# Optimization experiments

Hardware: AMD Instinct MI355X
Metric: run time of the kernel (lower is better)

The kernel has to match this reference:

```python
import jax, jax.numpy as jnp
import numpy as np

POOL = 7; SR = 2; SCALE = 1.0 / 16
NUM_CLASSES = 21
NMS_THR = 0.5; MIN_SIZE = 1.0; TOPK = 100; SCORE_THR = 0.05
BBOX_CLIP = float(np.log(1000.0 / 16))


def roi_align(feat, rois):
    # feat: [C,H,W]; rois: [P,4] xyxy in image coords. torchvision aligned=True, sampling_ratio=2.
    C, H, W = feat.shape
    S = POOL * SR
    x0r = rois[:, 0] * SCALE - 0.5
    y0r = rois[:, 1] * SCALE - 0.5
    bw = (rois[:, 2] - rois[:, 0]) * SCALE / POOL
    bh = (rois[:, 3] - rois[:, 1]) * SCALE / POOL
    t = (jnp.arange(S, dtype=feat.dtype) + 0.5) / SR  # sample offsets in bin units
    ys = y0r[:, None] + bh[:, None] * t  # [P,S]
    xs = x0r[:, None] + bw[:, None] * t  # [P,S]
    vy = (ys >= -1.0) & (ys <= H)
    vx = (xs >= -1.0) & (xs <= W)
    y = jnp.clip(ys, 0.0, H - 1)
    x = jnp.clip(xs, 0.0, W - 1)
    yl = jnp.floor(y).astype(jnp.int32); xl = jnp.floor(x).astype(jnp.int32)
    yh = jnp.minimum(yl + 1, H - 1);     xh = jnp.minimum(xl + 1, W - 1)
    ly = y - yl; lx = x - xl
    hy = 1.0 - ly; hx = 1.0 - lx

    def g(Yi, Xi):  # -> [C,P,S,S]
        return feat[:, Yi[:, :, None], Xi[:, None, :]]

    val = (g(yl, xl) * (hy[:, :, None] * hx[:, None, :])
         + g(yl, xh) * (hy[:, :, None] * lx[:, None, :])
         + g(yh, xl) * (ly[:, :, None] * hx[:, None, :])
         + g(yh, xh) * (ly[:, :, None] * lx[:, None, :]))
    val = val * (vy[:, :, None] & vx[:, None, :])[None].astype(feat.dtype)
    P = rois.shape[0]
    val = val.reshape(C, P, POOL, SR, POOL, SR).mean(axis=(3, 5))  # avg over 2x2 samples/bin
    return val.transpose(1, 0, 2, 3)  # [P,C,POOL,POOL]


def decode(pred, proposals):
    # pred: [N,K,4] (dx,dy,dw,dh); proposals: [N,4]
    w = proposals[:, 2] - proposals[:, 0]
    h = proposals[:, 3] - proposals[:, 1]
    cx = proposals[:, 0] + 0.5 * w
    cy = proposals[:, 1] + 0.5 * h
    dx, dy = pred[..., 0], pred[..., 1]
    dw = jnp.minimum(pred[..., 2], BBOX_CLIP)
    dh = jnp.minimum(pred[..., 3], BBOX_CLIP)
    pcx = dx * w[:, None] + cx[:, None]
    pcy = dy * h[:, None] + cy[:, None]
    pw = jnp.exp(dw) * w[:, None]
    ph = jnp.exp(dh) * h[:, None]
    return jnp.stack([pcx - 0.5 * pw, pcy - 0.5 * ph, pcx + 0.5 * pw, pcy + 0.5 * ph], axis=-1)


def box_iou(b):
    x1, y1, x2, y2 = b[:, 0], b[:, 1], b[:, 2], b[:, 3]
    area = (x2 - x1) * (y2 - y1)
    iw = jnp.maximum(jnp.minimum(x2[:, None], x2[None, :]) - jnp.maximum(x1[:, None], x1[None, :]), 0.0)
    ih = jnp.maximum(jnp.minimum(y2[:, None], y2[None, :]) - jnp.maximum(y1[:, None], y1[None, :]), 0.0)
    inter = iw * ih
    return inter / (area[:, None] + area[None, :] - inter)


def filter_predictions(boxes, labels, scores):
    # score threshold + min-size + per-class greedy NMS + topK, static shapes (padded to TOPK)
    N = scores.shape[0]
    ws = boxes[:, 2] - boxes[:, 0]
    hs = boxes[:, 3] - boxes[:, 1]
    valid = (scores > SCORE_THR) & (ws >= MIN_SIZE) & (hs >= MIN_SIZE)
    skey = jnp.where(valid, scores, -jnp.inf)
    order = jnp.argsort(-skey)
    b = boxes[order]; s = skey[order]; l = labels[order]; v = valid[order]
    # batched_nms via per-class coordinate offset
    off = jax.lax.stop_gradient(jnp.max(boxes) + 1.0)
    ob = jax.lax.stop_gradient(b) + (l.astype(b.dtype) * off)[:, None]
    iou = box_iou(ob)  # [N,N]
    idx = jnp.arange(N)

    def body(keep, i):
        sup = (iou[i] > NMS_THR) & keep[i] & (idx > i)
        return keep & ~sup, None

    keep, _ = jax.lax.scan(body, v, idx)
    rank = jnp.cumsum(keep) - 1
    final = keep & (rank < TOPK)
    pick = jnp.argsort(jnp.where(final, idx, N))[:TOPK]  # kept indices in score order, padded
    ok = final[pick]
    out_boxes = jnp.where(ok[:, None], b[pick], 0.0)
    out_scores = jnp.where(ok, s[pick], 0.0)
    out_labels = jnp.where(ok, l[pick], -1)
    return out_boxes, out_labels, out_scores


def roi_head_forward(image, feat, proposals, fc6_w, fc6_b, fc7_w, fc7_b, cls_w, cls_b, reg_w, reg_b):
    H_img, W_img = image.shape[-2], image.shape[-1]
    pooled = roi_align(feat[0], proposals)  # [P,C,7,7]
    x = pooled.reshape(pooled.shape[0], -1)
    x = jax.nn.relu(x @ fc6_w.T + fc6_b)
    x = jax.nn.relu(x @ fc7_w.T + fc7_b)
    cls_scores = x @ cls_w.T + cls_b                       # [P,K]
    box_pred = (x @ reg_w.T + reg_b).reshape(-1, NUM_CLASSES, 4)
    boxes = decode(box_pred, proposals)                    # [P,K,4]
    scores = jax.nn.softmax(cls_scores, axis=-1)
    boxes = jnp.stack([boxes[..., 0].clip(0, W_img), boxes[..., 1].clip(0, H_img),
                       boxes[..., 2].clip(0, W_img), boxes[..., 3].clip(0, H_img)], axis=-1)
    labels = jnp.broadcast_to(jnp.arange(NUM_CLASSES), scores.shape)
    boxes = boxes[:, 1:].reshape(-1, 4)
    scores = scores[:, 1:].reshape(-1)
    labels = (labels[:, 1:] - 1).reshape(-1)
    return filter_predictions(boxes, labels, scores)


def setup_inputs() -> dict:
    key = jax.random.key(0)
    ks = jax.random.split(key, 12)
    H_img, W_img = 800, 1072
    P, C = 300, 512
    image = jnp.zeros((1, 3, H_img, W_img), jnp.float32)
    feat = jax.random.normal(ks[0], (1, C, H_img // 16, W_img // 16), jnp.float32)
    cx = jax.random.uniform(ks[1], (P,)) * W_img
    cy = jax.random.uniform(ks[2], (P,)) * H_img
    bw = 20.0 + jax.random.uniform(ks[3], (P,)) * 300.0
    bh = 20.0 + jax.random.uniform(ks[4], (P,)) * 300.0
    proposals = jnp.stack([jnp.clip(cx - bw / 2, 0, W_img), jnp.clip(cy - bh / 2, 0, H_img),
                           jnp.clip(cx + bw / 2, 0, W_img), jnp.clip(cy + bh / 2, 0, H_img)], axis=1)
    fin = C * POOL * POOL  # 25088
    D = 1024
    fc6_w = jax.random.normal(ks[5], (D, fin), jnp.float32) / np.sqrt(fin)
    fc6_b = jnp.zeros((D,), jnp.float32)
    fc7_w = jax.random.normal(ks[6], (D, D), jnp.float32) / np.sqrt(D)
    fc7_b = jnp.zeros((D,), jnp.float32)
    cls_w = jax.random.normal(ks[7], (NUM_CLASSES, D), jnp.float32) / np.sqrt(D)
    cls_b = jnp.zeros((NUM_CLASSES,), jnp.float32)
    reg_w = jax.random.normal(ks[8], (NUM_CLASSES * 4, D), jnp.float32) * 0.001
    reg_b = jnp.zeros((NUM_CLASSES * 4,), jnp.float32)
    return {"image": image, "feat": feat, "proposals": proposals,
            "fc6_w": fc6_w, "fc6_b": fc6_b, "fc7_w": fc7_w, "fc7_b": fc7_b,
            "cls_w": cls_w, "cls_b": cls_b, "reg_w": reg_w, "reg_b": reg_b}


def reference(image, feat, proposals, fc6_w, fc6_b, fc7_w, fc7_b, cls_w, cls_b, reg_w, reg_b):
    return roi_head_forward(image, feat, proposals, fc6_w, fc6_b, fc7_w, fc7_b, cls_w, cls_b, reg_w, reg_b)
```

## Files before the change

kernel.cpp:

```cpp
#include <hip/hip_runtime.h>
#include <hip/hip_bf16.h>
#include <math.h>

#define P_N   300
#define C_N   512
#define H_F   50
#define W_F   67
#define HW_F  3350
#define D_N   1024
#define FIN   25088
#define NCLS  21
#define NCAND 6000
#define W_IMG 1072.0f
#define H_IMG 800.0f
#define BBOX_CLIP_F 4.135166556742356f
#define KS6   40
#define STEPS6_PER_Z 20
#define KS7   16
#define STEPS7_PER_Z 2
#define KSH   16
#define STEPSH_PER_Z 2
#define NHEAD 128
#define NW    96
#define A_SCALE 16.0f
#define B_SCALE 256.0f
#define O_SCALE (1.0f / 4096.0f)
#define TBLK  1680

typedef __attribute__((ext_vector_type(8)))  _Float16 half8;
typedef __attribute__((ext_vector_type(16))) float    f32x16;

__device__ __forceinline__ void splitA(float f, _Float16& h, _Float16& l) {
  float fs = f * A_SCALE;
  h = (_Float16)fs;
  l = (_Float16)(fs - (float)h);
}

__global__ __launch_bounds__(256) void prep_transpose(const float* __restrict__ feat,
                                                      float* __restrict__ ft,
                                                      const float* __restrict__ cls_w,
                                                      const float* __restrict__ cls_b,
                                                      const float* __restrict__ reg_w,
                                                      const float* __restrict__ reg_b,
                                                      float* __restrict__ Wpad,
                                                      float* __restrict__ bpad,
                                                      int* __restrict__ vcount) {
  __shared__ float tile[32][33];
  const int bid = blockIdx.x;
  const int tid = threadIdx.x;
  if (bid < TBLK) {
    const int bx = bid % 105, byy = bid / 105;
    const int s0 = bx * 32, c0 = byy * 32;
    const int tx = tid & 31, ty = tid >> 5;
    for (int r = ty; r < 32; r += 8) {
      int c = c0 + r, s = s0 + tx;
      tile[r][tx] = (s < HW_F) ? feat[(size_t)c * HW_F + s] : 0.0f;
    }
    __syncthreads();
    for (int r = ty; r < 32; r += 8) {
      int s = s0 + r, c = c0 + tx;
      if (s < HW_F) ft[(size_t)s * C_N + c] = tile[tx][r];
    }
  } else {
    const int row = bid - TBLK;
    if (row == 0 && tid == 0) *vcount = 0;
    const float* src = (row < NCLS) ? (cls_w + (size_t)row * D_N)
                     : (row < 105)  ? (reg_w + (size_t)(row - NCLS) * D_N) : nullptr;
    float4 v = make_float4(0.f, 0.f, 0.f, 0.f);
    if (src) v = reinterpret_cast<const float4*>(src)[tid];
    reinterpret_cast<float4*>(Wpad + (size_t)row * D_N)[tid] = v;
    if (tid == 0)
      bpad[row] = (row < NCLS) ? cls_b[row] : (row < 105) ? reg_b[row - NCLS] : 0.0f;
  }
}

__global__ __launch_bounds__(256) void roi_align_k(const float* __restrict__ ft,
                                                   const float* __restrict__ rois,
                                                   _Float16* __restrict__ Xhi,
                                                   _Float16* __restrict__ Xlo) {
  __shared__ _Float16 hbuf[12544] __attribute__((aligned(16)));
  __shared__ _Float16 lbuf[12544] __attribute__((aligned(16)));
  __shared__ int   g_yl[14], g_yh[14], g_xl[14], g_xh[14];
  __shared__ float g_ly[14], g_hy[14], g_lx[14], g_hx[14];
  __shared__ int   g_vy[14], g_vx[14];

  const int p   = blockIdx.x;
  const int ch  = blockIdx.y;
  const int tid = threadIdx.x;

  if (tid < 14) {
    const float rx0 = rois[p*4+0], ry0 = rois[p*4+1], rx1 = rois[p*4+2], ry1 = rois[p*4+3];
    const float x0r = rx0 * 0.0625f - 0.5f;
    const float y0r = ry0 * 0.0625f - 0.5f;
    const float bw  = (rx1 - rx0) * 0.0625f * (1.0f / 7.0f);
    const float bh  = (ry1 - ry0) * 0.0625f * (1.0f / 7.0f);
    const float t   = ((float)tid + 0.5f) * 0.5f;

    const float ys = y0r + bh * t;
    g_vy[tid] = (ys >= -1.0f) && (ys <= (float)H_F);
    float y = fminf(fmaxf(ys, 0.0f), (float)(H_F - 1));
    int yi = (int)floorf(y);
    g_yl[tid] = yi; g_yh[tid] = min(yi + 1, H_F - 1);
    g_ly[tid] = y - (float)yi; g_hy[tid] = 1.0f - (y - (float)yi);

    const float xs = x0r + bw * t;
    g_vx[tid] = (xs >= -1.0f) && (xs <= (float)W_F);
    float x = fminf(fmaxf(xs, 0.0f), (float)(W_F - 1));
    int xi = (int)floorf(x);
    g_xl[tid] = xi; g_xh[tid] = min(xi + 1, W_F - 1);
    g_lx[tid] = x - (float)xi; g_hx[tid] = 1.0f - (x - (float)xi);
  }
  __syncthreads();

  const int c = ch * 256 + tid;
  for (int cell = 0; cell < 49; ++cell) {
    const int py = cell / 7;
    const int px = cell - py * 7;
    float acc = 0.0f;
#pragma unroll
    for (int sy = 0; sy < 2; ++sy) {
      const int iy = 2 * py + sy;
      if (!g_vy[iy]) continue;
      const float ly = g_ly[iy], hy = g_hy[iy];
      const int ry0i = g_yl[iy] * W_F, ry1i = g_yh[iy] * W_F;
#pragma unroll
      for (int sx = 0; sx < 2; ++sx) {
        const int ix = 2 * px + sx;
        if (!g_vx[ix]) continue;
        const float lx = g_lx[ix], hx = g_hx[ix];
        const float* b00 = ft + (size_t)(ry0i + g_xl[ix]) * C_N;
        const float* b01 = ft + (size_t)(ry0i + g_xh[ix]) * C_N;
        const float* b10 = ft + (size_t)(ry1i + g_xl[ix]) * C_N;
        const float* b11 = ft + (size_t)(ry1i + g_xh[ix]) * C_N;
        acc += (hy*hx)*b00[c] + (hy*lx)*b01[c] + (ly*hx)*b10[c] + (ly*lx)*b11[c];
      }
    }
    _Float16 h, l;
    splitA(acc * 0.25f, h, l);
    hbuf[tid * 49 + cell] = h;
    lbuf[tid * 49 + cell] = l;
  }
  __syncthreads();

  const size_t base = (size_t)p * FIN + (size_t)ch * 12544;
  const uint4* hs = (const uint4*)hbuf;
  const uint4* ls = (const uint4*)lbuf;
  uint4* dh = (uint4*)(Xhi + base);
  uint4* dl = (uint4*)(Xlo + base);
  for (int k = tid; k < 1568; k += 256) { dh[k] = hs[k]; dl[k] = ls[k]; }
}

__device__ __forceinline__ int swz(int slot, int ks) {
  return slot ^ ((slot >> 5) & 1) ^ (((slot >> 3) & 1) << 1) ^ ((ks & 1) << 2);
}

__global__ __launch_bounds__(256, 3) void gemm_f16_3p(
    const _Float16* __restrict__ Ahi, const _Float16* __restrict__ Alo,
    const float* __restrict__ Wt, float* __restrict__ Pt,
    int M, int K, int steps_per_z, int ldc)
{
  __shared__ _Float16 lds[20480];
  const int tid  = threadIdx.x;
  const int lane = tid & 63, wave = tid >> 6;
  const int wm = wave >> 1, wn = wave & 1;

  const int GX = gridDim.x, GY = gridDim.y;
  const int T  = GX * GY * gridDim.z;
  int flat = blockIdx.x + GX * (blockIdx.y + GY * blockIdx.z);
  if ((T & 7) == 0) flat = (flat & 7) * (T >> 3) + (flat >> 3);
  const int bx = flat % GX;
  const int by = (flat / GX) % GY;
  const int bz = flat / (GX * GY);

  const int m0 = bx * 192, n0 = by * 128;
  const int steps_total = K >> 5;
  const int s0 = bz * steps_per_z;
  const int s1 = min(s0 + steps_per_z, steps_total);

  f32x16 acc[3][2];
#pragma unroll
  for (int a = 0; a < 3; ++a)
#pragma unroll
    for (int b = 0; b < 2; ++b)
#pragma unroll
      for (int r = 0; r < 16; ++r) acc[a][b][r] = 0.f;

  const int srow = tid >> 2;
  const int j8   = tid & 3;
  const int ksW  = j8 >> 1, kc8 = j8 & 1;
  const int wslot = swz((kc8 << 5) | (srow & 31), ksW);

  for (int step = s0; step < s1; ++step) {
    const int kb = step << 5;
#pragma unroll
    for (int half = 0; half < 3; ++half) {
      const int row = srow + half * 64;
      const int mf  = row >> 5;
      const int gm  = m0 + row;
      uint4 vh = make_uint4(0,0,0,0), vl = make_uint4(0,0,0,0);
      if (gm < M) {
        vh = *reinterpret_cast<const uint4*>(Ahi + (size_t)gm * K + kb + j8 * 8);
        vl = *reinterpret_cast<const uint4*>(Alo + (size_t)gm * K + kb + j8 * 8);
      }
      const int base = (mf * 2 + ksW) * 512 + wslot * 8;
      *reinterpret_cast<uint4*>(&lds[base])        = vh;
      *reinterpret_cast<uint4*>(&lds[6144 + base]) = vl;
    }
#pragma unroll
    for (int half = 0; half < 2; ++half) {
      const int n = srow + half * 64;
      const float* wp = Wt + (size_t)(n0 + n) * K + kb + j8 * 8;
      const float4 f0 = *reinterpret_cast<const float4*>(wp);
      const float4 f1 = *reinterpret_cast<const float4*>(wp + 4);
      float fv[8] = {f0.x, f0.y, f0.z, f0.w, f1.x, f1.y, f1.z, f1.w};
      union { _Float16 h[8]; uint4 v; } uh, ul;
#pragma unroll
      for (int e = 0; e < 8; ++e) {
        float fs = fv[e] * B_SCALE;
        uh.h[e] = (_Float16)fs;
        ul.h[e] = (_Float16)(fs - (float)uh.h[e]);
      }
      const int nf = n >> 5;
      const int base = 12288 + (nf * 2 + ksW) * 512 + wslot * 8;
      *reinterpret_cast<uint4*>(&lds[base])        = uh.v;
      *reinterpret_cast<uint4*>(&lds[4096 + base]) = ul.v;
    }
    __syncthreads();
#pragma unroll
    for (int ks = 0; ks < 2; ++ks) {
      const int rslot = swz(lane, ks) * 8;
      half8 ah[3], al[3], bh[2], bl[2];
#pragma unroll
      for (int mi = 0; mi < 3; ++mi) {
        const int mf = wm * 3 + mi;
        ah[mi] = *reinterpret_cast<const half8*>(&lds[(mf * 2 + ks) * 512 + rslot]);
        al[mi] = *reinterpret_cast<const half8*>(&lds[6144 + (mf * 2 + ks) * 512 + rslot]);
      }
#pragma unroll
      for (int ni = 0; ni < 2; ++ni) {
        const int nf = wn * 2 + ni;
        bh[ni] = *reinterpret_cast<const half8*>(&lds[12288 + (nf * 2 + ks) * 512 + rslot]);
        bl[ni] = *reinterpret_cast<const half8*>(&lds[16384 + (nf * 2 + ks) * 512 + rslot]);
      }
#pragma unroll
      for (int mi = 0; mi < 3; ++mi)
#pragma unroll
        for (int ni = 0; ni < 2; ++ni) {
          acc[mi][ni] = __builtin_amdgcn_mfma_f32_32x32x16_f16(ah[mi], bh[ni], acc[mi][ni], 0, 0, 0);
          acc[mi][ni] = __builtin_amdgcn_mfma_f32_32x32x16_f16(ah[mi], bl[ni], acc[mi][ni], 0, 0, 0);
          acc[mi][ni] = __builtin_amdgcn_mfma_f32_32x32x16_f16(al[mi], bh[ni], acc[mi][ni], 0, 0, 0);
        }
    }
    __syncthreads();
  }
  const int col = lane & 31, rhi = lane >> 5;
  float* outp = Pt + (size_t)bz * ((size_t)M * ldc);
#pragma unroll
  for (int mi = 0; mi < 3; ++mi)
#pragma unroll
    for (int ni = 0; ni < 2; ++ni) {
      const int n = n0 + (wn * 2 + ni) * 32 + col;
      if (n >= ldc) continue;
#pragma unroll
      for (int r = 0; r < 16; ++r) {
        const int m = m0 + (wm * 3 + mi) * 32 + ((r & 3) + 8 * (r >> 2) + 4 * rhi);
        if (m < M) outp[(size_t)m * ldc + n] = acc[mi][ni][r] * O_SCALE;
      }
    }
}

__global__ __launch_bounds__(256) void reduce_bias(
    const float* __restrict__ Pt, const float* __restrict__ bias,
    float* __restrict__ out_f32, _Float16* __restrict__ out_hi, _Float16* __restrict__ out_lo,
    int MN, int KS, int nmask, int relu)
{
  int i = blockIdx.x * 256 + threadIdx.x;
  if (i >= MN) return;
  float s = 0.0f;
  for (int k = 0; k < KS; ++k) s += Pt[(size_t)k * MN + i];
  s += bias[i & nmask];
  if (relu) s = fmaxf(s, 0.0f);
  if (out_f32) out_f32[i] = s;
  if (out_hi) {
    _Float16 h, l; splitA(s, h, l);
    out_hi[i] = h; out_lo[i] = l;
  }
}

__global__ __launch_bounds__(64) void decode_kernel(const float* __restrict__ logits,
                                                    const float* __restrict__ props,
                                                    float* __restrict__ cboxes,
                                                    unsigned long long* __restrict__ ckeys,
                                                    int* __restrict__ vcount) {
  const int p = blockIdx.x;
  const int lane = threadIdx.x;
  const float* lg = logits + (size_t)p * NHEAD;

  float s = (lane < NCLS) ? lg[lane] : -__builtin_inff();
  float mx = s;
#pragma unroll
  for (int off = 32; off > 0; off >>= 1) mx = fmaxf(mx, __shfl_xor(mx, off));
  float e = (lane < NCLS) ? expf(s - mx) : 0.0f;
  float sum = e;
#pragma unroll
  for (int off = 32; off > 0; off >>= 1) sum += __shfl_xor(sum, off);
  const float sm = e / sum;

  if (lane >= 1 && lane < NCLS) {
    const int c = lane;
    const float x0 = props[p*4+0], y0 = props[p*4+1], x1 = props[p*4+2], y1 = props[p*4+3];
    const float w = x1 - x0, hh = y1 - y0;
    const float cx = x0 + 0.5f * w, cy = y0 + 0.5f * hh;
    const float dx = lg[NCLS + c*4 + 0];
    const float dy = lg[NCLS + c*4 + 1];
    const float dw = fminf(lg[NCLS + c*4 + 2], BBOX_CLIP_F);
    const float dh = fminf(lg[NCLS + c*4 + 3], BBOX_CLIP_F);
    const float pcx = dx * w + cx, pcy = dy * hh + cy;
    const float pw = expf(dw) * w, ph = expf(dh) * hh;
    float bx0 = pcx - 0.5f * pw, by0 = pcy - 0.5f * ph;
    float bx1 = pcx + 0.5f * pw, by1 = pcy + 0.5f * ph;
    bx0 = fminf(fmaxf(bx0, 0.0f), W_IMG);
    by0 = fminf(fmaxf(by0, 0.0f), H_IMG);
    bx1 = fminf(fmaxf(bx1, 0.0f), W_IMG);
    by1 = fminf(fmaxf(by1, 0.0f), H_IMG);
    const int idx = p * 20 + (c - 1);
    cboxes[idx*4+0] = bx0; cboxes[idx*4+1] = by0;
    cboxes[idx*4+2] = bx1; cboxes[idx*4+3] = by1;
    const bool valid = (sm > 0.05f) && ((bx1 - bx0) >= 1.0f) && ((by1 - by0) >= 1.0f);
    if (valid) {
      int pos = atomicAdd(vcount, 1);
      unsigned u = __float_as_uint(sm);
      ckeys[pos] = ((unsigned long long)(~u) << 32) | (unsigned)idx;
    }
  }
}

__global__ __launch_bounds__(1024) void sort_gather(const unsigned long long* __restrict__ ckeys,
                                                    const int* __restrict__ vcount,
                                                    const float* __restrict__ cboxes,
                                                    float4* __restrict__ sbox,
                                                    float* __restrict__ sscore,
                                                    int* __restrict__ slab) {
  __shared__ unsigned long long keys[8192];
  const int tid = threadIdx.x;
  const int V = *vcount;
  int Npad = 64; while (Npad < V) Npad <<= 1;
  for (int i = tid; i < Npad; i += 1024)
    keys[i] = (i < V) ? ckeys[i] : ~0ULL;
  __syncthreads();
  for (int kk = 2; kk <= Npad; kk <<= 1) {
    for (int j = kk >> 1; j > 0; j >>= 1) {
      for (int i = tid; i < Npad; i += 1024) {
        int ij = i ^ j;
        if (ij > i) {
          unsigned long long a = keys[i], b = keys[ij];
          bool up = ((i & kk) == 0);
          if ((a > b) == up) { keys[i] = b; keys[ij] = a; }
        }
      }
      __syncthreads();
    }
  }
  for (int i = tid; i < V; i += 1024) {
    unsigned long long key = keys[i];
    int idx = (int)(key & 0xffffffffu);
    sbox[i]   = *reinterpret_cast<const float4*>(&cboxes[(size_t)idx * 4]);
    sscore[i] = __uint_as_float(~(unsigned)(key >> 32));
    slab[i]   = idx % 20;
  }
}

__global__ __launch_bounds__(256) void iou_matrix(const float4* __restrict__ sbox,
                                                  const int* __restrict__ slab,
                                                  const int* __restrict__ vcount,
                                                  unsigned long long* __restrict__ mask) {
  const int V = *vcount;
  const int i = blockIdx.x * 4 + (threadIdx.x >> 6);
  const int lane = threadIdx.x & 63;
  if (i >= V) return;
  const float4 bi = sbox[i];
  const int li = slab[i];
  const float ai = (bi.z - bi.x) * (bi.w - bi.y);
  const int nw = (V + 63) >> 6;
  for (int w = 0; w < nw; ++w) {
    const int j = (w << 6) + lane;
    bool sup = false;
    if (j > i && j < V && slab[j] == li) {
      const float4 bj = sbox[j];
      const float iw = fminf(bi.z, bj.z) - fmaxf(bi.x, bj.x);
      const float ih = fminf(bi.w, bj.w) - fmaxf(bi.y, bj.y);
      const float inter = fmaxf(iw, 0.0f) * fmaxf(ih, 0.0f);
      const float aj = (bj.z - bj.x) * (bj.w - bj.y);
      sup = inter / (ai + aj - inter) > 0.5f;
    }
    const unsigned long long m = __ballot(sup);
    if (lane == 0) mask[(size_t)i * NW + w] = m;
  }
}

__device__ __forceinline__ unsigned long long bcast_live(unsigned long long live0,
                                                         unsigned long long live1, int w) {
  union { unsigned long long u; uint2 v; } t;
  t.u = (w < 64) ? live0 : live1;
  const int src = w & 63;
  const unsigned lo = __shfl(t.v.x, src);
  const unsigned hi = __shfl(t.v.y, src);
  return ((unsigned long long)hi << 32) | lo;
}

__global__ __launch_bounds__(64) void nms_scan(const float4* __restrict__ sbox,
                                               const float* __restrict__ sscore,
                                               const int* __restrict__ slab,
                                               const int* __restrict__ vcount,
                                               const unsigned long long* __restrict__ mask,
                                               float* __restrict__ out) {
  const int lane = threadIdx.x;
  const int V = min(*vcount, NCAND);
  const int nw = (V + 63) >> 6;
  unsigned long long live0 = ~0ULL, live1 = ~0ULL;
  int nk = 0;
  for (int w = 0; w < nw && nk < 100; ++w) {
    const int nb = V - (w << 6);
    const unsigned long long vmask = (nb >= 64) ? ~0ULL : ((1ULL << nb) - 1ULL);
    unsigned long long wv = bcast_live(live0, live1, w) & vmask;
    while (wv && nk < 100) {
      const int b = __ffsll((long long)wv) - 1;
      const int i = (w << 6) + b;
      if (lane == 0) {
        const float4 bb = sbox[i];
        out[nk*4+0] = bb.x; out[nk*4+1] = bb.y; out[nk*4+2] = bb.z; out[nk*4+3] = bb.w;
        out[400 + nk] = (float)slab[i];
        out[500 + nk] = sscore[i];
      }
      const unsigned long long* mrow = mask + (size_t)i * NW;
      if (lane < nw) live0 &= ~mrow[lane];
      if (64 + lane < nw) live1 &= ~mrow[64 + lane];
      nk++;
      wv = bcast_live(live0, live1, w) & vmask;
      wv &= (b == 63) ? 0ULL : ~((2ULL << b) - 1ULL);
    }
  }
  for (int r = nk + lane; r < 100; r += 64) {
    out[r*4+0] = 0.0f; out[r*4+1] = 0.0f; out[r*4+2] = 0.0f; out[r*4+3] = 0.0f;
    out[400 + r] = -1.0f;
    out[500 + r] = 0.0f;
  }
}

extern "C" void kernel_launch(void* const* d_in, const int* in_sizes, int n_in,
                              void* d_out, int out_size, void* d_ws, size_t ws_size,
                              hipStream_t stream) {
  const float* feat   = (const float*)d_in[1];
  const float* props  = (const float*)d_in[2];
  const float* fc6_w  = (const float*)d_in[3];
  const float* fc6_b  = (const float*)d_in[4];
  const float* fc7_w  = (const float*)d_in[5];
  const float* fc7_b  = (const float*)d_in[6];
  const float* cls_w  = (const float*)d_in[7];
  const float* cls_b  = (const float*)d_in[8];
  const float* reg_w  = (const float*)d_in[9];
  const float* reg_b  = (const float*)d_in[10];

  char* ws = (char*)d_ws;
  size_t off = 0;
  auto alloc = [&](size_t bytes) -> void* {
    void* p = ws + off;
    off += (bytes + 255) & ~(size_t)255;
    return p;
  };

  _Float16* Xhi  = (_Float16*)alloc((size_t)P_N * FIN * 2);
  _Float16* Xlo  = (_Float16*)alloc((size_t)P_N * FIN * 2);
  float*    Pt   = (float*)alloc((size_t)KS6 * P_N * D_N * 4);
  _Float16* h6hi = (_Float16*)alloc((size_t)P_N * D_N * 2);
  _Float16* h6lo = (_Float16*)alloc((size_t)P_N * D_N * 2);
  _Float16* h7hi = (_Float16*)alloc((size_t)P_N * D_N * 2);
  _Float16* h7lo = (_Float16*)alloc((size_t)P_N * D_N * 2);
  float*    Wpad = (float*)alloc((size_t)NHEAD * D_N * 4);
  float*    bpad = (float*)alloc((size_t)NHEAD * 4);
  float*  logits = (float*)alloc((size_t)P_N * NHEAD * 4);
  float*  cboxes = (float*)alloc((size_t)NCAND * 4 * 4);
  unsigned long long* ckeys = (unsigned long long*)alloc((size_t)NCAND * 8);
  float4*   sbox = (float4*)alloc((size_t)NCAND * 16);
  float*  sscore = (float*)alloc((size_t)NCAND * 4);
  int*      slab = (int*)alloc((size_t)NCAND * 4);
  unsigned long long* supmask = (unsigned long long*)alloc((size_t)NCAND * NW * 8);
  int*    vcount = (int*)alloc(256);
  float* ft = Pt;
  (void)ws_size; (void)in_sizes; (void)n_in; (void)out_size;

  prep_transpose<<<TBLK + NHEAD, 256, 0, stream>>>(feat, ft, cls_w, cls_b, reg_w, reg_b,
                                                   Wpad, bpad, vcount);
  roi_align_k<<<dim3(P_N, 2), 256, 0, stream>>>(ft, props, Xhi, Xlo);
  gemm_f16_3p<<<dim3(2, 8, KS6), 256, 0, stream>>>(Xhi, Xlo, fc6_w, Pt, P_N, FIN, STEPS6_PER_Z, D_N);
  reduce_bias<<<(P_N * D_N + 255) / 256, 256, 0, stream>>>(
      Pt, fc6_b, nullptr, h6hi, h6lo, P_N * D_N, KS6, D_N - 1, 1);
  gemm_f16_3p<<<dim3(2, 8, KS7), 256, 0, stream>>>(h6hi, h6lo, fc7_w, Pt, P_N, D_N, STEPS7_PER_Z, D_N);
  reduce_bias<<<(P_N * D_N + 255) / 256, 256, 0, stream>>>(
      Pt, fc7_b, nullptr, h7hi, h7lo, P_N * D_N, KS7, D_N - 1, 1);
  gemm_f16_3p<<<dim3(2, 1, KSH), 256, 0, stream>>>(h7hi, h7lo, Wpad, Pt, P_N, D_N, STEPSH_PER_Z, NHEAD);
  reduce_bias<<<(P_N * NHEAD + 255) / 256, 256, 0, stream>>>(
      Pt, bpad, logits, nullptr, nullptr, P_N * NHEAD, KSH, NHEAD - 1, 0);
  decode_kernel<<<P_N, 64, 0, stream>>>(logits, props, cboxes, ckeys, vcount);
  sort_gather<<<1, 1024, 0, stream>>>(ckeys, vcount, cboxes, sbox, sscore, slab);
  iou_matrix<<<(NCAND + 3) / 4, 256, 0, stream>>>(sbox, slab, vcount, supmask);
  nms_scan<<<1, 64, 0, stream>>>(sbox, sscore, slab, vcount, supmask, (float*)d_out);
}
```

Before: 343.9 us.

## Pre-swizzle GEMM A operands into LDS-ready blobs and load via global_load_lds

Adds a reshuffle kernel that packs the ROI-aligned fp16 hi/lo activations into per-tile, per-k-step 16KB blobs already in the swizzled LDS layout. The GEMM then copies A straight into LDS with global_load_lds instead of doing per-thread loads and stores. The reduction kernels for fc6 and fc7 now write their outputs directly in this blob format. The M tile shrinks from 192 to 128 (a 3-wide grid), fc6 split-K goes from 40 to 28 slices, and the workspace is reorganised so buffers alias. The cost is an extra reshuffle pass over the roughly 30MB activation buffer, plus fewer accumulators per wave.

```diff
diff --git a/kernel.cpp b/kernel.cpp
--- a/kernel.cpp
+++ b/kernel.cpp
@@ -14,8 +14,8 @@
 #define W_IMG 1072.0f
 #define H_IMG 800.0f
 #define BBOX_CLIP_F 4.135166556742356f
-#define KS6   40
-#define STEPS6_PER_Z 20
+#define KS6   28
+#define STEPS6_PER_Z 28
 #define KS7   16
 #define STEPS7_PER_Z 2
 #define KSH   16
@@ -34,6 +34,16 @@
   float fs = f * A_SCALE;
   h = (_Float16)fs;
   l = (_Float16)(fs - (float)h);
+}
+
+__device__ __forceinline__ int swz(int slot, int ks) {
+  return slot ^ ((slot >> 5) & 1) ^ (((slot >> 3) & 1) << 1) ^ ((ks & 1) << 2);
+}
+
+__device__ __forceinline__ int blob_half_idx(int row, int j8) {
+  const int ksW = j8 >> 1, kc8 = j8 & 1;
+  const int mf = row >> 5;
+  return (mf * 2 + ksW) * 512 + swz((kc8 << 5) | (row & 31), ksW) * 8;
 }
 
 __global__ __launch_bounds__(256) void prep_transpose(const float* __restrict__ feat,
@@ -150,16 +160,40 @@
   for (int k = tid; k < 1568; k += 256) { dh[k] = hs[k]; dl[k] = ls[k]; }
 }
 
-__device__ __forceinline__ int swz(int slot, int ks) {
-  return slot ^ ((slot >> 5) & 1) ^ (((slot >> 3) & 1) << 1) ^ ((ks & 1) << 2);
+__global__ __launch_bounds__(256) void reshuffle_x(const _Float16* __restrict__ Shi,
+                                                   const _Float16* __restrict__ Slo,
+                                                   char* __restrict__ blob,
+                                                   int M2, int K) {
+  __shared__ _Float16 buf[8192] __attribute__((aligned(16)));
+  const int tile = blockIdx.x, step = blockIdx.y;
+  const int tid = threadIdx.x;
+  const int steps = K >> 5;
+#pragma unroll
+  for (int i = 0; i < 4; ++i) {
+    const int g = tid + i * 256;
+    const int half = g >> 9;
+    const int row = (g >> 2) & 127;
+    const int j8 = g & 3;
+    const int gm = tile * 128 + row;
+    uint4 v = make_uint4(0, 0, 0, 0);
+    if (gm < M2) {
+      const _Float16* src = (half ? Slo : Shi) + (size_t)gm * K + (step << 5) + (j8 << 3);
+      v = *reinterpret_cast<const uint4*>(src);
+    }
+    *reinterpret_cast<uint4*>(buf + half * 4096 + blob_half_idx(row, j8)) = v;
+  }
+  __syncthreads();
+  uint4* dst = (uint4*)(blob + (((size_t)tile * steps + step) << 14));
+  const uint4* s = (const uint4*)buf;
+#pragma unroll
+  for (int i = 0; i < 4; ++i) dst[tid + i * 256] = s[tid + i * 256];
 }
 
 __global__ __launch_bounds__(256, 3) void gemm_f16_3p(
-    const _Float16* __restrict__ Ahi, const _Float16* __restrict__ Alo,
-    const float* __restrict__ Wt, float* __restrict__ Pt,
+    const char* __restrict__ Ablob, const float* __restrict__ Wt, float* __restrict__ Pt,
     int M, int K, int steps_per_z, int ldc)
 {
-  __shared__ _Float16 lds[20480];
+  __shared__ _Float16 lds[16384] __attribute__((aligned(16)));
   const int tid  = threadIdx.x;
   const int lane = tid & 63, wave = tid >> 6;
   const int wm = wave >> 1, wn = wave & 1;
@@ -172,14 +206,14 @@
   const int by = (flat / GX) % GY;
   const int bz = flat / (GX * GY);
 
-  const int m0 = bx * 192, n0 = by * 128;
+  const int m0 = bx * 128, n0 = by * 128;
   const int steps_total = K >> 5;
   const int s0 = bz * steps_per_z;
   const int s1 = min(s0 + steps_per_z, steps_total);
 
-  f32x16 acc[3][2];
-#pragma unroll
-  for (int a = 0; a < 3; ++a)
+  f32x16 acc[2][2];
+#pragma unroll
+  for (int a = 0; a < 2; ++a)
 #pragma unroll
     for (int b = 0; b < 2; ++b)
 #pragma unroll
@@ -192,19 +226,14 @@
 
   for (int step = s0; step < s1; ++step) {
     const int kb = step << 5;
-#pragma unroll
-    for (int half = 0; half < 3; ++half) {
-      const int row = srow + half * 64;
-      const int mf  = row >> 5;
-      const int gm  = m0 + row;
-      uint4 vh = make_uint4(0,0,0,0), vl = make_uint4(0,0,0,0);
-      if (gm < M) {
-        vh = *reinterpret_cast<const uint4*>(Ahi + (size_t)gm * K + kb + j8 * 8);
-        vl = *reinterpret_cast<const uint4*>(Alo + (size_t)gm * K + kb + j8 * 8);
-      }
-      const int base = (mf * 2 + ksW) * 512 + wslot * 8;
-      *reinterpret_cast<uint4*>(&lds[base])        = vh;
-      *reinterpret_cast<uint4*>(&lds[6144 + base]) = vl;
+    const char* Ab = Ablob + (((size_t)bx * steps_total + step) << 14);
+#pragma unroll
+    for (int c2 = 0; c2 < 4; ++c2) {
+      const int off = ((wave << 2) + c2) << 10;
+      __builtin_amdgcn_global_load_lds(
+          (const __attribute__((address_space(1))) uint32_t*)(Ab + off + (lane << 4)),
+          (__attribute__((address_space(3))) uint32_t*)((char*)lds + off),
+          16, 0, 0);
     }
 #pragma unroll
     for (int half = 0; half < 2; ++half) {
@@ -221,7 +250,7 @@
         ul.h[e] = (_Float16)(fs - (float)uh.h[e]);
       }
       const int nf = n >> 5;
-      const int base = 12288 + (nf * 2 + ksW) * 512 + wslot * 8;
+      const int base = 8192 + (nf * 2 + ksW) * 512 + wslot * 8;
       *reinterpret_cast<uint4*>(&lds[base])        = uh.v;
       *reinterpret_cast<uint4*>(&lds[4096 + base]) = ul.v;
     }
@@ -229,21 +258,21 @@
 #pragma unroll
     for (int ks = 0; ks < 2; ++ks) {
       const int rslot = swz(lane, ks) * 8;
-      half8 ah[3], al[3], bh[2], bl[2];
-#pragma unroll
-      for (int mi = 0; mi < 3; ++mi) {
-        const int mf = wm * 3 + mi;
+      half8 ah[2], al[2], bh[2], bl[2];
+#pragma unroll
+      for (int mi = 0; mi < 2; ++mi) {
+        const int mf = wm * 2 + mi;
         ah[mi] = *reinterpret_cast<const half8*>(&lds[(mf * 2 + ks) * 512 + rslot]);
-        al[mi] = *reinterpret_cast<const half8*>(&lds[6144 + (mf * 2 + ks) * 512 + rslot]);
+        al[mi] = *reinterpret_cast<const half8*>(&lds[4096 + (mf * 2 + ks) * 512 + rslot]);
       }
 #pragma unroll
       for (int ni = 0; ni < 2; ++ni) {
         const int nf = wn * 2 + ni;
-        bh[ni] = *reinterpret_cast<const half8*>(&lds[12288 + (nf * 2 + ks) * 512 + rslot]);
-        bl[ni] = *reinterpret_cast<const half8*>(&lds[16384 + (nf * 2 + ks) * 512 + rslot]);
-      }
-#pragma unroll
-      for (int mi = 0; mi < 3; ++mi)
+        bh[ni] = *reinterpret_cast<const half8*>(&lds[8192  + (nf * 2 + ks) * 512 + rslot]);
+        bl[ni] = *reinterpret_cast<const half8*>(&lds[12288 + (nf * 2 + ks) * 512 + rslot]);
+      }
+#pragma unroll
+      for (int mi = 0; mi < 2; ++mi)
 #pragma unroll
         for (int ni = 0; ni < 2; ++ni) {
           acc[mi][ni] = __builtin_amdgcn_mfma_f32_32x32x16_f16(ah[mi], bh[ni], acc[mi][ni], 0, 0, 0);
@@ -256,35 +285,63 @@
   const int col = lane & 31, rhi = lane >> 5;
   float* outp = Pt + (size_t)bz * ((size_t)M * ldc);
 #pragma unroll
-  for (int mi = 0; mi < 3; ++mi)
+  for (int mi = 0; mi < 2; ++mi)
 #pragma unroll
     for (int ni = 0; ni < 2; ++ni) {
       const int n = n0 + (wn * 2 + ni) * 32 + col;
       if (n >= ldc) continue;
 #pragma unroll
       for (int r = 0; r < 16; ++r) {
-        const int m = m0 + (wm * 3 + mi) * 32 + ((r & 3) + 8 * (r >> 2) + 4 * rhi);
+        const int m = m0 + (wm * 2 + mi) * 32 + ((r & 3) + 8 * (r >> 2) + 4 * rhi);
         if (m < M) outp[(size_t)m * ldc + n] = acc[mi][ni][r] * O_SCALE;
       }
     }
 }
 
-__global__ __launch_bounds__(256) void reduce_bias(
-    const float* __restrict__ Pt, const float* __restrict__ bias,
-    float* __restrict__ out_f32, _Float16* __restrict__ out_hi, _Float16* __restrict__ out_lo,
-    int MN, int KS, int nmask, int relu)
-{
+__global__ __launch_bounds__(256) void reduce_frag(const float* __restrict__ Pt,
+                                                   const float* __restrict__ bias,
+                                                   char* __restrict__ blob,
+                                                   int KS, int stepsB) {
+  const int g = blockIdx.x * 256 + threadIdx.x;
+  if (g >= P_N * 128) return;
+  const int m = g >> 7;
+  const int gg = g & 127;
+  const int n0 = gg << 3;
+  float s[8];
+#pragma unroll
+  for (int e = 0; e < 8; ++e) s[e] = bias[n0 + e];
+  for (int k2 = 0; k2 < KS; ++k2) {
+    const float* pp = Pt + ((size_t)k2 * P_N + m) * D_N + n0;
+    const float4 a = *reinterpret_cast<const float4*>(pp);
+    const float4 b = *reinterpret_cast<const float4*>(pp + 4);
+    s[0]+=a.x; s[1]+=a.y; s[2]+=a.z; s[3]+=a.w;
+    s[4]+=b.x; s[5]+=b.y; s[6]+=b.z; s[7]+=b.w;
+  }
+  union { _Float16 h[8]; uint4 v; } uh, ul;
+#pragma unroll
+  for (int e = 0; e < 8; ++e) {
+    float r = fmaxf(s[e], 0.0f);
+    _Float16 h, l; splitA(r, h, l);
+    uh.h[e] = h; ul.h[e] = l;
+  }
+  const int tile = m >> 7, row = m & 127;
+  const int step = gg >> 2, j8 = gg & 3;
+  _Float16* dst = (_Float16*)(blob + (((size_t)tile * stepsB + step) << 14));
+  const int hidx = blob_half_idx(row, j8);
+  *reinterpret_cast<uint4*>(dst + hidx) = uh.v;
+  *reinterpret_cast<uint4*>(dst + 4096 + hidx) = ul.v;
+}
+
+__global__ __launch_bounds__(256) void reduce_bias(const float* __restrict__ Pt,
+                                                   const float* __restrict__ bias,
+                                                   float* __restrict__ out_f32,
+                                                   int MN, int KS, int nmask) {
   int i = blockIdx.x * 256 + threadIdx.x;
   if (i >= MN) return;
   float s = 0.0f;
   for (int k = 0; k < KS; ++k) s += Pt[(size_t)k * MN + i];
   s += bias[i & nmask];
-  if (relu) s = fmaxf(s, 0.0f);
-  if (out_f32) out_f32[i] = s;
-  if (out_hi) {
-    _Float16 h, l; splitA(s, h, l);
-    out_hi[i] = h; out_lo[i] = l;
-  }
+  out_f32[i] = s;
 }
 
 __global__ __launch_bounds__(64) void decode_kernel(const float* __restrict__ logits,
@@ -462,45 +519,46 @@
   const float* reg_b  = (const float*)d_in[10];
 
   char* ws = (char*)d_ws;
-  size_t off = 0;
+  const size_t XSZ = (size_t)P_N * FIN * 2;
+  const size_t R1  = (size_t)KS6 * P_N * D_N * 4;
+  _Float16* Xhi = (_Float16*)ws;
+  _Float16* Xlo = (_Float16*)(ws + XSZ);
+  float*    Pt  = (float*)ws;
+  char* reg2 = ws + R1;
+  float* ft   = (float*)reg2;
+  char*  Xb   = reg2;
+  const size_t XBSZ = (size_t)3 * 784 * 16384;
+  size_t off = R1 + XBSZ;
   auto alloc = [&](size_t bytes) -> void* {
     void* p = ws + off;
     off += (bytes + 255) & ~(size_t)255;
     return p;
   };
-
-  _Float16* Xhi  = (_Float16*)alloc((size_t)P_N * FIN * 2);
-  _Float16* Xlo  = (_Float16*)alloc((size_t)P_N * FIN * 2);
-  float*    Pt   = (float*)alloc((size_t)KS6 * P_N * D_N * 4);
-  _Float16* h6hi = (_Float16*)alloc((size_t)P_N * D_N * 2);
-  _Float16* h6lo = (_Float16*)alloc((size_t)P_N * D_N * 2);
-  _Float16* h7hi = (_Float16*)alloc((size_t)P_N * D_N * 2);
-  _Float16* h7lo = (_Float16*)alloc((size_t)P_N * D_N * 2);
-  float*    Wpad = (float*)alloc((size_t)NHEAD * D_N * 4);
-  float*    bpad = (float*)alloc((size_t)NHEAD * 4);
-  float*  logits = (float*)alloc((size_t)P_N * NHEAD * 4);
-  float*  cboxes = (float*)alloc((size_t)NCAND * 4 * 4);
+  char*  h6b   = (char*)alloc((size_t)3 * 32 * 16384);
+  char*  h7b   = (char*)alloc((size_t)3 * 32 * 16384);
+  float* Wpad  = (float*)alloc((size_t)NHEAD * D_N * 4);
+  float* bpad  = (float*)alloc((size_t)NHEAD * 4);
+  float* logits= (float*)alloc((size_t)P_N * NHEAD * 4);
+  float* cboxes= (float*)alloc((size_t)NCAND * 4 * 4);
   unsigned long long* ckeys = (unsigned long long*)alloc((size_t)NCAND * 8);
-  float4*   sbox = (float4*)alloc((size_t)NCAND * 16);
-  float*  sscore = (float*)alloc((size_t)NCAND * 4);
-  int*      slab = (int*)alloc((size_t)NCAND * 4);
+  float4* sbox = (float4*)alloc((size_t)NCAND * 16);
+  float* sscore= (float*)alloc((size_t)NCAND * 4);
+  int*   slab  = (int*)alloc((size_t)NCAND * 4);
   unsigned long long* supmask = (unsigned long long*)alloc((size_t)NCAND * NW * 8);
-  int*    vcount = (int*)alloc(256);
-  float* ft = Pt;
+  int*   vcount= (int*)alloc(256);
   (void)ws_size; (void)in_sizes; (void)n_in; (void)out_size;
 
   prep_transpose<<<TBLK + NHEAD, 256, 0, stream>>>(feat, ft, cls_w, cls_b, reg_w, reg_b,
                                                    Wpad, bpad, vcount);
   roi_align_k<<<dim3(P_N, 2), 256, 0, stream>>>(ft, props, Xhi, Xlo);
-  gemm_f16_3p<<<dim3(2, 8, KS6), 256, 0, stream>>>(Xhi, Xlo, fc6_w, Pt, P_N, FIN, STEPS6_PER_Z, D_N);
-  reduce_bias<<<(P_N * D_N + 255) / 256, 256, 0, stream>>>(
-      Pt, fc6_b, nullptr, h6hi, h6lo, P_N * D_N, KS6, D_N - 1, 1);
-  gemm_f16_3p<<<dim3(2, 8, KS7), 256, 0, stream>>>(h6hi, h6lo, fc7_w, Pt, P_N, D_N, STEPS7_PER_Z, D_N);
-  reduce_bias<<<(P_N * D_N + 255) / 256, 256, 0, stream>>>(
-      Pt, fc7_b, nullptr, h7hi, h7lo, P_N * D_N, KS7, D_N - 1, 1);
-  gemm_f16_3p<<<dim3(2, 1, KSH), 256, 0, stream>>>(h7hi, h7lo, Wpad, Pt, P_N, D_N, STEPSH_PER_Z, NHEAD);
+  reshuffle_x<<<dim3(3, 784), 256, 0, stream>>>(Xhi, Xlo, Xb, P_N, FIN);
+  gemm_f16_3p<<<dim3(3, 8, KS6), 256, 0, stream>>>(Xb, fc6_w, Pt, P_N, FIN, STEPS6_PER_Z, D_N);
+  reduce_frag<<<150, 256, 0, stream>>>(Pt, fc6_b, h6b, KS6, 32);
+  gemm_f16_3p<<<dim3(3, 8, KS7), 256, 0, stream>>>(h6b, fc7_w, Pt, P_N, D_N, STEPS7_PER_Z, D_N);
+  reduce_frag<<<150, 256, 0, stream>>>(Pt, fc7_b, h7b, KS7, 32);
+  gemm_f16_3p<<<dim3(3, 1, KSH), 256, 0, stream>>>(h7b, Wpad, Pt, P_N, D_N, STEPSH_PER_Z, NHEAD);
   reduce_bias<<<(P_N * NHEAD + 255) / 256, 256, 0, stream>>>(
-      Pt, bpad, logits, nullptr, nullptr, P_N * NHEAD, KSH, NHEAD - 1, 0);
+      Pt, bpad, logits, P_N * NHEAD, KSH, NHEAD - 1);
   decode_kernel<<<P_N, 64, 0, stream>>>(logits, props, cboxes, ckeys, vcount);
   sort_gather<<<1, 1024, 0, stream>>>(ckeys, vcount, cboxes, sbox, sscore, slab);
   iou_matrix<<<(NCAND + 3) / 4, 256, 0, stream>>>(sbox, slab, vcount, supmask);
```

Result: no change. 346.0 us (+0.6%).
